# Optimization experiments

Measured on AMD Instinct MI355X. Metric: run time of the kernel, lower is better.

The kernel has to match this reference:

```python
import jax, jax.numpy as jnp
import numpy as np

B, N, E, IN_DIM, OUT_DIM = 8, 4500, 72000, 128, 128
EPS = 1e-5  # torch LayerNorm default


def setup_inputs() -> dict:
    key = jax.random.key(0)
    k0, k1, k2 = jax.random.split(key, 3)
    node_features = jax.random.normal(k0, (B, N, IN_DIM), dtype=jnp.float32)
    edge_index = jax.random.randint(k1, (B, 2, E), 0, N, dtype=jnp.int64)
    node_mask = jnp.ones((B, N), dtype=jnp.float32)
    edge_mask = jnp.ones((B, E), dtype=jnp.float32)
    W = (jax.random.normal(k2, (OUT_DIM, IN_DIM), dtype=jnp.float32)
         / np.float32(np.sqrt(IN_DIM)))
    b = jnp.zeros((OUT_DIM,), dtype=jnp.float32)
    gamma = jnp.ones((OUT_DIM,), dtype=jnp.float32)
    beta = jnp.zeros((OUT_DIM,), dtype=jnp.float32)
    return {"node_features": node_features, "edge_index": edge_index,
            "node_mask": node_mask, "edge_mask": edge_mask,
            "W": W, "b": b, "gamma": gamma, "beta": beta}


def reference(node_features, edge_index, node_mask, edge_mask, W, b, gamma, beta):
    Bsz, Nn, _ = node_features.shape
    # linear transform: h = x W^T + b  -> [B, N, out_dim]
    h = jnp.einsum('bni,oi->bno', node_features, W) + b
    D = h.shape[-1]
    total = Bsz * Nn

    # With all nodes valid, the sparse index of node (b, n) is b*Nn + n.
    offsets = (jnp.arange(Bsz, dtype=edge_index.dtype) * Nn)[:, None]  # [B,1]
    src = (edge_index[:, 0, :] + offsets).reshape(-1)  # [B*E]
    tgt = (edge_index[:, 1, :] + offsets).reshape(-1)  # [B*E]
    ew = edge_mask.reshape(-1)                          # [B*E] edge validity

    flat_h = h.reshape(total, D)

    # in-degree (valid edges only) + self-loop, D^{-1/2} normalization
    deg = jax.ops.segment_sum(ew, tgt, num_segments=total) + 1.0
    dinv = deg ** -0.5

    coef = dinv[src] * dinv[tgt] * ew                   # [B*E]
    msg = flat_h[src] * coef[:, None]                   # gather + weight
    agg = jax.ops.segment_sum(msg, tgt, num_segments=total)
    agg = agg + flat_h * dinv[:, None]                  # self contribution

    h = h + agg.reshape(Bsz, Nn, D)                     # residual

    # dropout is identity at inference; LayerNorm then ReLU then mask
    mu = jnp.mean(h, axis=-1, keepdims=True)
    var = jnp.mean((h - mu) ** 2, axis=-1, keepdims=True)
    h = (h - mu) / jnp.sqrt(var + EPS) * gamma + beta
    h = jax.nn.relu(h) * node_mask[..., None]
    return h
```

## Files before the change

kernel.cpp:

```cpp
#include <hip/hip_runtime.h>
#include <math.h>

typedef unsigned short ushort_t;
typedef unsigned int uint_t;
typedef __attribute__((ext_vector_type(8))) short bf16x8;
typedef __attribute__((ext_vector_type(16))) float f32x16;

constexpr int Bc   = 8;
constexpr int Nn   = 4500;
constexpr int Ec   = 72000;
constexpr int D    = 128;
constexpr int T    = Bc * Nn;
constexpr int TE   = Bc * Ec;
constexpr float EPS = 1e-5f;

constexpr int PAD = 32;
constexpr int RST = 64;

constexpr int NB_PREP = (T * PAD / 4) / 256;

constexpr int NB_ECH  = (Ec + 255) / 256;
constexpr int NB_EDGE = 8 * NB_ECH;

constexpr int NB_GEMM = ((T / 32) * 2 + 3) / 4;
constexpr int NB_DINV = 8 * 18;
constexpr int NB_GD   = NB_GEMM + NB_DINV;

constexpr size_t WS_CNTP  = 0;
constexpr size_t WS_EDATA = 4608000;
constexpr size_t WS_DINV  = 13824000;
constexpr size_t WS_H     = 13968000;

__device__ __forceinline__ ushort_t f32_to_bf16_rne(float f) {
  uint_t u = __float_as_uint(f);
  uint_t r = (u + 0x7fffu + ((u >> 16) & 1u)) >> 16;
  return (ushort_t)r;
}
__device__ __forceinline__ float bf16_to_f32(ushort_t h) {
  return __uint_as_float(((uint_t)h) << 16);
}

__global__ __launch_bounds__(256) void prep_kernel(int4* __restrict__ cntp4) {
  int i = blockIdx.x * 256 + threadIdx.x;
  cntp4[i] = make_int4(0, 0, 0, 0);
}

__global__ __launch_bounds__(256) void edge_kernel(
    const int* __restrict__ ei, const float* __restrict__ em,
    int* __restrict__ cntp, uint_t* __restrict__ edata) {
  const int b  = blockIdx.x & 7;
  const int el = (blockIdx.x >> 3) * 256 + threadIdx.x;
  if (el >= Ec) return;
  const int* eb = ei + b * 2 * Ec;
  int t0 = eb[Ec + el];
  if ((unsigned)t0 >= (unsigned)Nn) return;
  int tg = t0 + b * Nn;
  int rk = atomicAdd(&cntp[(size_t)tg * PAD], 1);
  if (rk >= RST) return;
  int s0 = eb[el];
  float ew = em[b * Ec + el];
  uint_t sl = (uint_t)s0;
  if ((unsigned)s0 >= (unsigned)Nn) { sl = 0; ew = 0.f; }
  uint_t pk = ((uint_t)f32_to_bf16_rne(ew) << 16) | sl;
  edata[(size_t)tg * RST + rk] = pk;
}

__global__ __launch_bounds__(256) void gemm_dinv_kernel(
    const float* __restrict__ x, const float* __restrict__ W,
    const float* __restrict__ bias, ushort_t* __restrict__ h,
    const uint_t* __restrict__ edata, const int* __restrict__ cntp,
    float* __restrict__ dinv) {
  const int bid = blockIdx.x;
  if (bid < NB_GEMM) {
    const int g = bid * 4 + (threadIdx.x >> 6);
    if (g >= (T / 32) * 2) return;
    const int lane = threadIdx.x & 63;
    const int mt = g >> 1;
    const int nh = g & 1;
    const int m0 = mt * 32;
    const int r  = lane & 31;
    const int kh = lane >> 5;

    const float* xrow = x + (size_t)(m0 + r) * D + kh * 8;

    f32x16 acc[2];
#pragma unroll
    for (int n = 0; n < 2; ++n)
#pragma unroll
      for (int j = 0; j < 16; ++j) acc[n][j] = 0.f;

#pragma unroll
    for (int ks = 0; ks < 8; ++ks) {
      const float4 p0 = ((const float4*)(xrow + ks * 16))[0];
      const float4 p1 = ((const float4*)(xrow + ks * 16))[1];
      const float xa[8] = {p0.x, p0.y, p0.z, p0.w, p1.x, p1.y, p1.z, p1.w};
      bf16x8 ahi, alo;
#pragma unroll
      for (int j = 0; j < 8; ++j) {
        ushort_t hb = f32_to_bf16_rne(xa[j]);
        ahi[j] = (short)hb;
        alo[j] = (short)f32_to_bf16_rne(xa[j] - bf16_to_f32(hb));
      }
#pragma unroll
      for (int n = 0; n < 2; ++n) {
        const float* wrow = W + (size_t)((nh * 2 + n) * 32 + r) * D
                              + ks * 16 + kh * 8;
        const float4 w0 = ((const float4*)wrow)[0];
        const float4 w1 = ((const float4*)wrow)[1];
        bf16x8 bhi;
        bhi[0] = (short)f32_to_bf16_rne(w0.x);
        bhi[1] = (short)f32_to_bf16_rne(w0.y);
        bhi[2] = (short)f32_to_bf16_rne(w0.z);
        bhi[3] = (short)f32_to_bf16_rne(w0.w);
        bhi[4] = (short)f32_to_bf16_rne(w1.x);
        bhi[5] = (short)f32_to_bf16_rne(w1.y);
        bhi[6] = (short)f32_to_bf16_rne(w1.z);
        bhi[7] = (short)f32_to_bf16_rne(w1.w);
        acc[n] = __builtin_amdgcn_mfma_f32_32x32x16_bf16(ahi, bhi, acc[n], 0, 0, 0);
        acc[n] = __builtin_amdgcn_mfma_f32_32x32x16_bf16(alo, bhi, acc[n], 0, 0, 0);
      }
    }

#pragma unroll
    for (int n = 0; n < 2; ++n) {
      const int col = (nh * 2 + n) * 32 + r;
      const float bv = bias[col];
#pragma unroll
      for (int j = 0; j < 16; ++j) {
        const int mrow = m0 + (j & 3) + 8 * (j >> 2) + 4 * kh;
        h[(size_t)mrow * D + col] = f32_to_bf16_rne(acc[n][j] + bv);
      }
    }
  } else {
    const int zb = bid - NB_GEMM;
    const int b  = zb & 7;
    const int nl = (zb >> 3) * 256 + threadIdx.x;
    if (nl >= Nn) return;
    const int i = b * Nn + nl;
    int cnt = cntp[(size_t)i * PAD];
    cnt = (cnt > RST) ? RST : cnt;
    const uint_t* row = edata + (size_t)i * RST;
    float s = 0.f;
    for (int j = 0; j < cnt; ++j) s += bf16_to_f32((ushort_t)(row[j] >> 16));
    dinv[i] = 1.0f / sqrtf(s + 1.0f);
  }
}

__global__ __launch_bounds__(256) void gather_ln_kernel(
    const ushort_t* __restrict__ h, const int* __restrict__ cntp,
    const uint_t* __restrict__ edata, const float* __restrict__ dinv,
    const float* __restrict__ gamma, const float* __restrict__ beta,
    const float* __restrict__ mask, float* __restrict__ out) {
  const int bid  = blockIdx.x;
  const int b    = bid & 7;
  const int wid  = threadIdx.x >> 6;
  const int node = b * Nn + (bid >> 3) * 4 + wid;
  const int bOff = b * Nn;
  const int lane = threadIdx.x & 63;
  const int f4   = lane & 31;
  const int half = lane >> 5;

  const ushort4* h4 = (const ushort4*)h;
  int cnt = cntp[(size_t)node * PAD];
  cnt = (cnt > RST) ? RST : cnt;
  const uint_t* row = edata + (size_t)node * RST;

  ushort4 hq = h4[(size_t)node * 32 + f4];
  float4 hv = make_float4(bf16_to_f32(hq.x), bf16_to_f32(hq.y),
                          bf16_to_f32(hq.z), bf16_to_f32(hq.w));

  float4 accE = make_float4(0.f, 0.f, 0.f, 0.f);
  int i = half;
  for (; i + 6 < cnt; i += 8) {
    uint_t p0 = row[i];
    uint_t p1 = row[i + 2];
    uint_t p2 = row[i + 4];
    uint_t p3 = row[i + 6];
    int sg0 = bOff + (p0 & 0xFFFFu);
    int sg1 = bOff + (p1 & 0xFFFFu);
    int sg2 = bOff + (p2 & 0xFFFFu);
    int sg3 = bOff + (p3 & 0xFFFFu);
    float c0 = dinv[sg0] * bf16_to_f32((ushort_t)(p0 >> 16));
    float c1 = dinv[sg1] * bf16_to_f32((ushort_t)(p1 >> 16));
    float c2 = dinv[sg2] * bf16_to_f32((ushort_t)(p2 >> 16));
    float c3 = dinv[sg3] * bf16_to_f32((ushort_t)(p3 >> 16));
    ushort4 q0 = h4[(size_t)sg0 * 32 + f4];
    ushort4 q1 = h4[(size_t)sg1 * 32 + f4];
    ushort4 q2 = h4[(size_t)sg2 * 32 + f4];
    ushort4 q3 = h4[(size_t)sg3 * 32 + f4];
    accE.x += bf16_to_f32(q0.x) * c0 + bf16_to_f32(q1.x) * c1 +
              bf16_to_f32(q2.x) * c2 + bf16_to_f32(q3.x) * c3;
    accE.y += bf16_to_f32(q0.y) * c0 + bf16_to_f32(q1.y) * c1 +
              bf16_to_f32(q2.y) * c2 + bf16_to_f32(q3.y) * c3;
    accE.z += bf16_to_f32(q0.z) * c0 + bf16_to_f32(q1.z) * c1 +
              bf16_to_f32(q2.z) * c2 + bf16_to_f32(q3.z) * c3;
    accE.w += bf16_to_f32(q0.w) * c0 + bf16_to_f32(q1.w) * c1 +
              bf16_to_f32(q2.w) * c2 + bf16_to_f32(q3.w) * c3;
  }
  for (; i < cnt; i += 2) {
    uint_t p0 = row[i];
    int sg0 = bOff + (p0 & 0xFFFFu);
    float c0 = dinv[sg0] * bf16_to_f32((ushort_t)(p0 >> 16));
    ushort4 q0 = h4[(size_t)sg0 * 32 + f4];
    accE.x += bf16_to_f32(q0.x) * c0;
    accE.y += bf16_to_f32(q0.y) * c0;
    accE.z += bf16_to_f32(q0.z) * c0;
    accE.w += bf16_to_f32(q0.w) * c0;
  }

  accE.x += __shfl_xor(accE.x, 32);
  accE.y += __shfl_xor(accE.y, 32);
  accE.z += __shfl_xor(accE.z, 32);
  accE.w += __shfl_xor(accE.w, 32);

  const float dt = dinv[node];
  float4 acc;
  acc.x = hv.x * (1.f + dt) + dt * accE.x;
  acc.y = hv.y * (1.f + dt) + dt * accE.y;
  acc.z = hv.z * (1.f + dt) + dt * accE.z;
  acc.w = hv.w * (1.f + dt) + dt * accE.w;

  float su = acc.x + acc.y + acc.z + acc.w;
  float ss = acc.x * acc.x + acc.y * acc.y + acc.z * acc.z + acc.w * acc.w;
#pragma unroll
  for (int o = 16; o > 0; o >>= 1) {
    su += __shfl_xor(su, o);
    ss += __shfl_xor(ss, o);
  }
  float mu  = su * (1.0f / 128.0f);
  float var = ss * (1.0f / 128.0f) - mu * mu;
  float rs  = 1.0f / sqrtf(var + EPS);
  float m   = mask[node];

  float4 g  = ((const float4*)gamma)[f4];
  float4 bb = ((const float4*)beta)[f4];
  float4 rv;
  rv.x = fmaxf((acc.x - mu) * rs * g.x + bb.x, 0.f) * m;
  rv.y = fmaxf((acc.y - mu) * rs * g.y + bb.y, 0.f) * m;
  rv.z = fmaxf((acc.z - mu) * rs * g.z + bb.z, 0.f) * m;
  rv.w = fmaxf((acc.w - mu) * rs * g.w + bb.w, 0.f) * m;
  if (half == 0) ((float4*)out)[(size_t)node * 32 + f4] = rv;
}

extern "C" void kernel_launch(void* const* d_in, const int* in_sizes, int n_in,
                              void* d_out, int out_size, void* d_ws, size_t ws_size,
                              hipStream_t stream) {
  const float* x     = (const float*)d_in[0];
  const int*   ei    = (const int*)d_in[1];
  const float* nmask = (const float*)d_in[2];
  const float* emask = (const float*)d_in[3];
  const float* W     = (const float*)d_in[4];
  const float* bias  = (const float*)d_in[5];
  const float* gamma = (const float*)d_in[6];
  const float* beta  = (const float*)d_in[7];
  float* out = (float*)d_out;

  char*     ws    = (char*)d_ws;
  int*      cntp  = (int*)     (ws + WS_CNTP);
  uint_t*   edata = (uint_t*)  (ws + WS_EDATA);
  float*    dinv  = (float*)   (ws + WS_DINV);
  ushort_t* h     = (ushort_t*)(ws + WS_H);

  prep_kernel<<<NB_PREP, 256, 0, stream>>>((int4*)cntp);
  edge_kernel<<<NB_EDGE, 256, 0, stream>>>(ei, emask, cntp, edata);
  gemm_dinv_kernel<<<NB_GD, 256, 0, stream>>>(x, W, bias, h,
                                              edata, cntp, dinv);
  gather_ln_kernel<<<T / 4, 256, 0, stream>>>(h, cntp, edata, dinv,
                                              gamma, beta, nmask, out);
}
```

Baseline: 80.25 us.

## Fuse zeroing into GEMM kernel and accumulate degree via atomics in edge pass

Merges the counter-zeroing prep kernel into the GEMM launch and drops the separate dinv pass. The edge kernel now atomically accumulates a padded per-node degree alongside the count, and the gather kernel computes rsqrt(deg+1) on the fly for each neighbor. This removes one kernel launch and the dinv rescan of edge data. In exchange it adds a second atomic per edge, doubles the zeroed region, and turns each dinv lookup in the gather into a strided padded load plus an rsqrt.

```diff
diff --git a/kernel.cpp b/kernel.cpp
--- a/kernel.cpp
+++ b/kernel.cpp
@@ -17,19 +17,18 @@
 constexpr int PAD = 32;
 constexpr int RST = 64;
 
-constexpr int NB_PREP = (T * PAD / 4) / 256;
+constexpr int NB_GEMM   = ((T / 32) * 2 + 3) / 4;
+constexpr int N_ZERO_I4 = (2 * T * PAD) / 4;
+constexpr int NB_ZERO   = N_ZERO_I4 / 256;
+constexpr int NB_K1     = NB_GEMM + NB_ZERO;
 
 constexpr int NB_ECH  = (Ec + 255) / 256;
 constexpr int NB_EDGE = 8 * NB_ECH;
 
-constexpr int NB_GEMM = ((T / 32) * 2 + 3) / 4;
-constexpr int NB_DINV = 8 * 18;
-constexpr int NB_GD   = NB_GEMM + NB_DINV;
-
 constexpr size_t WS_CNTP  = 0;
-constexpr size_t WS_EDATA = 4608000;
-constexpr size_t WS_DINV  = 13824000;
-constexpr size_t WS_H     = 13968000;
+constexpr size_t WS_DEGP  = 4608000;
+constexpr size_t WS_EDATA = 9216000;
+constexpr size_t WS_H     = 18432000;
 
 __device__ __forceinline__ ushort_t f32_to_bf16_rne(float f) {
   uint_t u = __float_as_uint(f);
@@ -40,36 +39,10 @@
   return __uint_as_float(((uint_t)h) << 16);
 }
 
-__global__ __launch_bounds__(256) void prep_kernel(int4* __restrict__ cntp4) {
-  int i = blockIdx.x * 256 + threadIdx.x;
-  cntp4[i] = make_int4(0, 0, 0, 0);
-}
-
-__global__ __launch_bounds__(256) void edge_kernel(
-    const int* __restrict__ ei, const float* __restrict__ em,
-    int* __restrict__ cntp, uint_t* __restrict__ edata) {
-  const int b  = blockIdx.x & 7;
-  const int el = (blockIdx.x >> 3) * 256 + threadIdx.x;
-  if (el >= Ec) return;
-  const int* eb = ei + b * 2 * Ec;
-  int t0 = eb[Ec + el];
-  if ((unsigned)t0 >= (unsigned)Nn) return;
-  int tg = t0 + b * Nn;
-  int rk = atomicAdd(&cntp[(size_t)tg * PAD], 1);
-  if (rk >= RST) return;
-  int s0 = eb[el];
-  float ew = em[b * Ec + el];
-  uint_t sl = (uint_t)s0;
-  if ((unsigned)s0 >= (unsigned)Nn) { sl = 0; ew = 0.f; }
-  uint_t pk = ((uint_t)f32_to_bf16_rne(ew) << 16) | sl;
-  edata[(size_t)tg * RST + rk] = pk;
-}
-
-__global__ __launch_bounds__(256) void gemm_dinv_kernel(
+__global__ __launch_bounds__(256) void gemm_zero_kernel(
     const float* __restrict__ x, const float* __restrict__ W,
     const float* __restrict__ bias, ushort_t* __restrict__ h,
-    const uint_t* __restrict__ edata, const int* __restrict__ cntp,
-    float* __restrict__ dinv) {
+    int4* __restrict__ zero4) {
   const int bid = blockIdx.x;
   if (bid < NB_GEMM) {
     const int g = bid * 4 + (threadIdx.x >> 6);
@@ -132,23 +105,36 @@
       }
     }
   } else {
-    const int zb = bid - NB_GEMM;
-    const int b  = zb & 7;
-    const int nl = (zb >> 3) * 256 + threadIdx.x;
-    if (nl >= Nn) return;
-    const int i = b * Nn + nl;
-    int cnt = cntp[(size_t)i * PAD];
-    cnt = (cnt > RST) ? RST : cnt;
-    const uint_t* row = edata + (size_t)i * RST;
-    float s = 0.f;
-    for (int j = 0; j < cnt; ++j) s += bf16_to_f32((ushort_t)(row[j] >> 16));
-    dinv[i] = 1.0f / sqrtf(s + 1.0f);
-  }
+    int i = (bid - NB_GEMM) * 256 + threadIdx.x;
+    zero4[i] = make_int4(0, 0, 0, 0);
+  }
+}
+
+__global__ __launch_bounds__(256) void edge_kernel(
+    const int* __restrict__ ei, const float* __restrict__ em,
+    int* __restrict__ cntp, float* __restrict__ degp,
+    uint_t* __restrict__ edata) {
+  const int b  = blockIdx.x & 7;
+  const int el = (blockIdx.x >> 3) * 256 + threadIdx.x;
+  if (el >= Ec) return;
+  const int* eb = ei + b * 2 * Ec;
+  int t0 = eb[Ec + el];
+  if ((unsigned)t0 >= (unsigned)Nn) return;
+  int tg = t0 + b * Nn;
+  float ew = em[b * Ec + el];
+  int rk = atomicAdd(&cntp[(size_t)tg * PAD], 1);
+  atomicAdd(&degp[(size_t)tg * PAD], ew);
+  if (rk >= RST) return;
+  int s0 = eb[el];
+  uint_t sl = (uint_t)s0;
+  if ((unsigned)s0 >= (unsigned)Nn) { sl = 0; ew = 0.f; }
+  uint_t pk = ((uint_t)f32_to_bf16_rne(ew) << 16) | sl;
+  edata[(size_t)tg * RST + rk] = pk;
 }
 
 __global__ __launch_bounds__(256) void gather_ln_kernel(
     const ushort_t* __restrict__ h, const int* __restrict__ cntp,
-    const uint_t* __restrict__ edata, const float* __restrict__ dinv,
+    const float* __restrict__ degp, const uint_t* __restrict__ edata,
     const float* __restrict__ gamma, const float* __restrict__ beta,
     const float* __restrict__ mask, float* __restrict__ out) {
   const int bid  = blockIdx.x;
@@ -180,10 +166,14 @@
     int sg1 = bOff + (p1 & 0xFFFFu);
     int sg2 = bOff + (p2 & 0xFFFFu);
     int sg3 = bOff + (p3 & 0xFFFFu);
-    float c0 = dinv[sg0] * bf16_to_f32((ushort_t)(p0 >> 16));
-    float c1 = dinv[sg1] * bf16_to_f32((ushort_t)(p1 >> 16));
-    float c2 = dinv[sg2] * bf16_to_f32((ushort_t)(p2 >> 16));
-    float c3 = dinv[sg3] * bf16_to_f32((ushort_t)(p3 >> 16));
+    float c0 = rsqrtf(degp[(size_t)sg0 * PAD] + 1.0f) *
+               bf16_to_f32((ushort_t)(p0 >> 16));
+    float c1 = rsqrtf(degp[(size_t)sg1 * PAD] + 1.0f) *
+               bf16_to_f32((ushort_t)(p1 >> 16));
+    float c2 = rsqrtf(degp[(size_t)sg2 * PAD] + 1.0f) *
+               bf16_to_f32((ushort_t)(p2 >> 16));
+    float c3 = rsqrtf(degp[(size_t)sg3 * PAD] + 1.0f) *
+               bf16_to_f32((ushort_t)(p3 >> 16));
     ushort4 q0 = h4[(size_t)sg0 * 32 + f4];
     ushort4 q1 = h4[(size_t)sg1 * 32 + f4];
     ushort4 q2 = h4[(size_t)sg2 * 32 + f4];
@@ -200,7 +190,8 @@
   for (; i < cnt; i += 2) {
     uint_t p0 = row[i];
     int sg0 = bOff + (p0 & 0xFFFFu);
-    float c0 = dinv[sg0] * bf16_to_f32((ushort_t)(p0 >> 16));
+    float c0 = rsqrtf(degp[(size_t)sg0 * PAD] + 1.0f) *
+               bf16_to_f32((ushort_t)(p0 >> 16));
     ushort4 q0 = h4[(size_t)sg0 * 32 + f4];
     accE.x += bf16_to_f32(q0.x) * c0;
     accE.y += bf16_to_f32(q0.y) * c0;
@@ -213,7 +204,7 @@
   accE.z += __shfl_xor(accE.z, 32);
   accE.w += __shfl_xor(accE.w, 32);
 
-  const float dt = dinv[node];
+  const float dt = rsqrtf(degp[(size_t)node * PAD] + 1.0f);
   float4 acc;
   acc.x = hv.x * (1.f + dt) + dt * accE.x;
   acc.y = hv.y * (1.f + dt) + dt * accE.y;
@@ -257,14 +248,12 @@
 
   char*     ws    = (char*)d_ws;
   int*      cntp  = (int*)     (ws + WS_CNTP);
+  float*    degp  = (float*)   (ws + WS_DEGP);
   uint_t*   edata = (uint_t*)  (ws + WS_EDATA);
-  float*    dinv  = (float*)   (ws + WS_DINV);
   ushort_t* h     = (ushort_t*)(ws + WS_H);
 
-  prep_kernel<<<NB_PREP, 256, 0, stream>>>((int4*)cntp);
-  edge_kernel<<<NB_EDGE, 256, 0, stream>>>(ei, emask, cntp, edata);
-  gemm_dinv_kernel<<<NB_GD, 256, 0, stream>>>(x, W, bias, h,
-                                              edata, cntp, dinv);
-  gather_ln_kernel<<<T / 4, 256, 0, stream>>>(h, cntp, edata, dinv,
+  gemm_zero_kernel<<<NB_K1, 256, 0, stream>>>(x, W, bias, h, (int4*)cntp);
+  edge_kernel<<<NB_EDGE, 256, 0, stream>>>(ei, emask, cntp, degp, edata);
+  gather_ln_kernel<<<T / 4, 256, 0, stream>>>(h, cntp, degp, edata,
                                               gamma, beta, nmask, out);
 }
```

New measurement: 105.6 us. 31.6% more time.
